# Performance work log

Measured on AMD Instinct MI355X. Metric: run time of the kernel, lower is better.

Reference implementation:

```python
import jax, jax.numpy as jnp
import numpy as np

TOP_K = 2


def setup_inputs() -> dict:
    key = jax.random.key(0)
    ks = jax.random.split(key, 6)
    B, S, H, I, E = 2, 1024, 1024, 2048, 8
    s_h = 1.0 / np.sqrt(H)
    s_i = 1.0 / np.sqrt(I)
    return {
        "x": jax.random.normal(ks[0], (B, S, H), jnp.float32),
        "gate_w": jax.random.normal(ks[1], (H, E), jnp.float32) * s_h,
        "gate_b": jnp.zeros((E,), jnp.float32),
        "w1": jax.random.normal(ks[2], (E, H, I), jnp.float32) * s_h,
        "w3": jax.random.normal(ks[3], (E, H, I), jnp.float32) * s_h,
        "w2": jax.random.normal(ks[4], (E, I, H), jnp.float32) * s_i,
    }


def reference(x, gate_w, gate_b, w1, w3, w2):
    # Gating: softmax over experts, then top-k selection + renormalization.
    logits = jnp.einsum("bsh,he->bse", x, gate_w) + gate_b            # [B,S,E]
    probs = jax.nn.softmax(logits, axis=-1)
    topk_w, topk_idx = jax.lax.top_k(probs, TOP_K)                    # [B,S,K]
    topk_w = topk_w / jnp.sum(topk_w, axis=-1, keepdims=True)

    E = gate_w.shape[-1]
    # Per-token combine weight for each expert (0 if not routed there).
    # one_hot: [B,S,K,E] -> combine: [B,S,E]
    combine = jnp.sum(jax.nn.one_hot(topk_idx, E, dtype=x.dtype) * topk_w[..., None], axis=-2)

    # SwiGLU expert FFN: down(silu(gate(x)) * up(x)); dense-masked reference
    # (compute every expert on every token, weight by combine; math identical
    # to the original gather/scatter loop since combine is 0 off-route).
    out = jnp.zeros_like(x)
    for e in range(E):
        h = jax.nn.silu(x @ w1[e]) * (x @ w3[e])                      # [B,S,I]
        out = out + combine[..., e:e + 1] * (h @ w2[e])               # [B,S,H]
    return out
```

## Files before the change

### kernel.cpp

```cpp
#include <hip/hip_runtime.h>
#include <hip/hip_bf16.h>
#include <math.h>

typedef __attribute__((ext_vector_type(4))) float f32x4;
typedef __attribute__((ext_vector_type(8))) short bf16x8;

#define T_TOK 2048
#define H_DIM 1024
#define I_DIM 2048
#define E_NUM 8

__device__ inline unsigned short f2bf(float f) {
  union { float f; unsigned int u; } v; v.f = f;
  unsigned int r = v.u + 0x7fffu + ((v.u >> 16) & 1u);
  return (unsigned short)(r >> 16);
}
__device__ inline unsigned int pack2(float a, float b) {
  return (unsigned int)f2bf(a) | ((unsigned int)f2bf(b) << 16);
}

__device__ inline void gld16(const void* g, void* l) {
  __builtin_amdgcn_global_load_lds((const __attribute__((address_space(1))) void*)g,
                                   (__attribute__((address_space(3))) void*)l, 16, 0, 0);
}

__device__ inline void transpose_pair(const float* __restrict__ ip, unsigned short* __restrict__ op,
                                      int R, int C, int rp, int ct, char* smem)
{
  unsigned short (*tl)[66] = (unsigned short (*)[66])smem;
  int r0 = rp * 128, c0 = ct * 64;
  int tid = threadIdx.x;
  int rq = (tid >> 4) * 4;
  int c4 = (tid & 15) * 4;
  const float* b0 = ip + (size_t)(r0 + rq) * C + c0 + c4;
  const float* b1 = b0 + (size_t)64 * C;
  float4 v[8];
  v[0] = *(const float4*)(b0);
  v[1] = *(const float4*)(b0 + C);
  v[2] = *(const float4*)(b0 + 2 * C);
  v[3] = *(const float4*)(b0 + 3 * C);
  v[4] = *(const float4*)(b1);
  v[5] = *(const float4*)(b1 + C);
  v[6] = *(const float4*)(b1 + 2 * C);
  v[7] = *(const float4*)(b1 + 3 * C);
  const float* f = (const float*)v;
#pragma unroll
  for (int j = 0; j < 4; ++j) {
    *(unsigned int*)&tl[c4 + j][rq]          = pack2(f[0 * 4 + j], f[1 * 4 + j]);
    *(unsigned int*)&tl[c4 + j][rq + 2]      = pack2(f[2 * 4 + j], f[3 * 4 + j]);
    *(unsigned int*)&tl[64 + c4 + j][rq]     = pack2(f[4 * 4 + j], f[5 * 4 + j]);
    *(unsigned int*)&tl[64 + c4 + j][rq + 2] = pack2(f[6 * 4 + j], f[7 * 4 + j]);
  }
  __syncthreads();
  int c = tid >> 3, r8 = (tid & 7) * 8;
#pragma unroll
  for (int it = 0; it < 2; ++it) {
    int cc = c + it * 32;
#pragma unroll
    for (int p = 0; p < 2; ++p) {
      uint4 o;
      o.x = *(const unsigned int*)&tl[p * 64 + cc][r8];
      o.y = *(const unsigned int*)&tl[p * 64 + cc][r8 + 2];
      o.z = *(const unsigned int*)&tl[p * 64 + cc][r8 + 4];
      o.w = *(const unsigned int*)&tl[p * 64 + cc][r8 + 6];
      *(uint4*)(op + (size_t)(c0 + cc) * R + r0 + p * 64 + r8) = o;
    }
  }
}

__global__ __launch_bounds__(256) void gate_t13(
    const float* __restrict__ x, const float* __restrict__ gw, const float* __restrict__ gb,
    int* __restrict__ rec_e, float* __restrict__ rec_w, unsigned short* __restrict__ xb,
    const float* __restrict__ w1, const float* __restrict__ w3,
    unsigned short* __restrict__ w1t, unsigned short* __restrict__ w3t)
{
  __shared__ __align__(16) char smem[128 * 66 * 2];
  int bx = blockIdx.x;
  if (bx >= 512) {
    int idx = bx - 512;
    int m = idx >> 8;
    int t8 = idx & 255;
    int rp = t8 & 7;
    int ct = t8 >> 3;
    const float* ip = (m < 8 ? w1 : w3) + (size_t)(m & 7) * ((size_t)H_DIM * I_DIM);
    unsigned short* op = (m < 8 ? w1t : w3t) + (size_t)(m & 7) * ((size_t)H_DIM * I_DIM);
    transpose_pair(ip, op, H_DIM, I_DIM, rp, ct, smem);
    return;
  }
  int wv = threadIdx.x >> 6, lane = threadIdx.x & 63;
  int t = bx * 4 + wv;
  const float* xr = x + (size_t)t * H_DIM;
  unsigned short* xo = xb + (size_t)t * H_DIM;
  float acc[8];
#pragma unroll
  for (int e = 0; e < 8; ++e) acc[e] = 0.f;
  for (int i = 0; i < H_DIM / 64; ++i) {
    int h = i * 64 + lane;
    float xv = xr[h];
    xo[h] = f2bf(xv);
    const float4* g = (const float4*)(gw + (size_t)h * 8);
    float4 g0 = g[0], g1 = g[1];
    acc[0] += xv * g0.x; acc[1] += xv * g0.y; acc[2] += xv * g0.z; acc[3] += xv * g0.w;
    acc[4] += xv * g1.x; acc[5] += xv * g1.y; acc[6] += xv * g1.z; acc[7] += xv * g1.w;
  }
#pragma unroll
  for (int s = 1; s < 64; s <<= 1) {
#pragma unroll
    for (int e = 0; e < 8; ++e) acc[e] += __shfl_xor(acc[e], s);
  }
  if (lane == 0) {
    float l[8];
#pragma unroll
    for (int e = 0; e < 8; ++e) l[e] = acc[e] + gb[e];
    int e0 = 0;
    for (int e = 1; e < 8; ++e) if (l[e] > l[e0]) e0 = e;
    int e1 = (e0 == 0) ? 1 : 0;
    for (int e = 0; e < 8; ++e) if (e != e0 && l[e] > l[e1]) e1 = e;
    float w0 = 1.f / (1.f + expf(l[e1] - l[e0]));
    rec_e[t * 2]     = e0; rec_e[t * 2 + 1] = e1;
    rec_w[t * 2]     = w0; rec_w[t * 2 + 1] = 1.f - w0;
  }
}

__global__ __launch_bounds__(256) void route8(
    const int* __restrict__ rec_e, const float* __restrict__ rec_w,
    int* __restrict__ counts_g, int* __restrict__ list_tok, float* __restrict__ list_w)
{
  __shared__ int cnt[8];
  __shared__ int fill;
  int e = blockIdx.x;
  int tid = threadIdx.x;
  if (tid < 8) cnt[tid] = 0;
  if (tid == 0) fill = 0;
  __syncthreads();
  int e_loc[16];
  int c_loc[8];
#pragma unroll
  for (int k = 0; k < 8; ++k) c_loc[k] = 0;
#pragma unroll
  for (int it = 0; it < 16; ++it) {
    e_loc[it] = rec_e[it * 256 + tid] & 7;
    c_loc[e_loc[it]]++;
  }
#pragma unroll
  for (int k = 0; k < 8; ++k) if (c_loc[k]) atomicAdd(&cnt[k], c_loc[k]);
  __syncthreads();
  if (e == 0 && tid < 8) counts_g[tid] = cnt[tid];
  int base = 0;
#pragma unroll
  for (int k = 0; k < 8; ++k) if (k < e) base += cnt[k];
#pragma unroll
  for (int it = 0; it < 16; ++it) {
    if (e_loc[it] == e) {
      int i = it * 256 + tid;
      int pos = atomicAdd(&fill, 1);
      list_tok[base + pos] = i;
      list_w[base + pos]   = rec_w[i];
    }
  }
}

__global__ __launch_bounds__(256, 2) void gemm1_t2(
    const unsigned short* __restrict__ xb,
    const unsigned short* __restrict__ w1t,
    const unsigned short* __restrict__ w3t,
    const int* __restrict__ counts,
    const int* __restrict__ list_tok,
    unsigned short* __restrict__ hbuf,
    const float* __restrict__ w2,
    unsigned short* __restrict__ w2t)
{
  __shared__ __align__(16) char smem[49152];
  int bx = blockIdx.x;
  if (bx >= 4096) {
    int idx = bx - 4096;
    int e = idx >> 8;
    int t8 = idx & 255;
    int rp = t8 & 15;
    int ct = t8 >> 4;
    const float* ip = w2 + (size_t)e * ((size_t)H_DIM * I_DIM);
    unsigned short* op = w2t + (size_t)e * ((size_t)H_DIM * I_DIM);
    transpose_pair(ip, op, I_DIM, H_DIM, rp, ct, smem);
    return;
  }
  int e = bx >> 9;
  int y = (bx >> 4) & 31;
  int ix = bx & 15;
  int nbase = 0;
#pragma unroll
  for (int i = 0; i < 8; ++i) if (i < e) nbase += counts[i];
  int n_e = counts[e];
  int t0 = y * 128;
  if (t0 >= n_e) return;
  int i0 = ix * 128;

  char* As  = smem;
  char* B1s = smem + 16384;
  char* B3s = smem + 32768;

  int tid = threadIdx.x;
  int r2 = tid >> 2;
  int seg = (tid & 3) * 8;

  int sr0 = t0 + r2;       if (sr0 >= n_e) sr0 = n_e - 1;
  int sr1 = t0 + 64 + r2;  if (sr1 >= n_e) sr1 = n_e - 1;
  int tok0 = list_tok[nbase + sr0] >> 1;
  int tok1 = list_tok[nbase + sr1] >> 1;
  const char* gA0 = (const char*)(xb + (size_t)tok0 * H_DIM + seg);
  const char* gA1 = (const char*)(xb + (size_t)tok1 * H_DIM + seg);
  const char* gB1a = (const char*)(w1t + ((size_t)e * I_DIM + i0 + r2) * H_DIM + seg);
  const char* gB1b = (const char*)(w1t + ((size_t)e * I_DIM + i0 + 64 + r2) * H_DIM + seg);
  const char* gB3a = (const char*)(w3t + ((size_t)e * I_DIM + i0 + r2) * H_DIM + seg);
  const char* gB3b = (const char*)(w3t + ((size_t)e * I_DIM + i0 + 64 + r2) * H_DIM + seg);

  int w = tid >> 6, lane = tid & 63, lm = lane & 15, lq = lane >> 4;
  int wm = w & 1, wn = w >> 1;

  f32x4 acc1[4][4], acc3[4][4];
#pragma unroll
  for (int i = 0; i < 4; ++i)
#pragma unroll
    for (int j = 0; j < 4; ++j) { acc1[i][j] = (f32x4){0,0,0,0}; acc3[i][j] = (f32x4){0,0,0,0}; }

  for (int kb = 0; kb < H_DIM; kb += 64) {
    __syncthreads();
    gld16(gA0 + kb * 2,       As + tid * 16);
    gld16(gA1 + kb * 2,       As + 4096 + tid * 16);
    gld16(gA0 + kb * 2 + 64,  As + 8192 + tid * 16);
    gld16(gA1 + kb * 2 + 64,  As + 12288 + tid * 16);
    gld16(gB1a + kb * 2,      B1s + tid * 16);
    gld16(gB1b + kb * 2,      B1s + 4096 + tid * 16);
    gld16(gB1a + kb * 2 + 64, B1s + 8192 + tid * 16);
    gld16(gB1b + kb * 2 + 64, B1s + 12288 + tid * 16);
    gld16(gB3a + kb * 2,      B3s + tid * 16);
    gld16(gB3b + kb * 2,      B3s + 4096 + tid * 16);
    gld16(gB3a + kb * 2 + 64, B3s + 8192 + tid * 16);
    gld16(gB3b + kb * 2 + 64, B3s + 12288 + tid * 16);
    __syncthreads();
#pragma unroll
    for (int s = 0; s < 2; ++s) {
      bf16x8 a[4], b1[4], b3[4];
#pragma unroll
      for (int i = 0; i < 4; ++i)
        a[i] = *(const bf16x8*)(As + s * 8192 + ((wm * 64 + i * 16 + lm) * 32 + lq * 8) * 2);
#pragma unroll
      for (int j = 0; j < 4; ++j) {
        b1[j] = *(const bf16x8*)(B1s + s * 8192 + ((wn * 64 + j * 16 + lm) * 32 + lq * 8) * 2);
        b3[j] = *(const bf16x8*)(B3s + s * 8192 + ((wn * 64 + j * 16 + lm) * 32 + lq * 8) * 2);
      }
#pragma unroll
      for (int i = 0; i < 4; ++i)
#pragma unroll
        for (int j = 0; j < 4; ++j) {
          acc1[i][j] = __builtin_amdgcn_mfma_f32_16x16x32_bf16(a[i], b1[j], acc1[i][j], 0, 0, 0);
          acc3[i][j] = __builtin_amdgcn_mfma_f32_16x16x32_bf16(a[i], b3[j], acc3[i][j], 0, 0, 0);
        }
    }
  }

#pragma unroll
  for (int i = 0; i < 4; ++i) {
#pragma unroll
    for (int rr = 0; rr < 4; ++rr) {
      int slot = t0 + wm * 64 + i * 16 + lq * 4 + rr;
      if (slot < n_e) {
        unsigned short* orow = hbuf + (size_t)(nbase + slot) * I_DIM + i0 + wn * 64 + lm;
#pragma unroll
        for (int j = 0; j < 4; ++j) {
          float g = acc1[i][j][rr], u = acc3[i][j][rr];
          float hv = (g / (1.f + __expf(-g))) * u;
          orow[j * 16] = f2bf(hv);
        }
      }
    }
  }
}

__global__ __launch_bounds__(256, 4) void gemm2(
    const unsigned short* __restrict__ hbuf,
    const unsigned short* __restrict__ w2t,
    const int* __restrict__ counts,
    const int* __restrict__ list_tok,
    const float* __restrict__ list_w,
    float* __restrict__ partial)
{
  __shared__ __align__(16) char smem[24576];
  int e = blockIdx.z;
  int nbase = 0;
#pragma unroll
  for (int i = 0; i < 8; ++i) if (i < e) nbase += counts[i];
  int n_e = counts[e];
  int ts = blockIdx.y >> 1, kh = blockIdx.y & 1;
  int t0 = ts * 64;
  if (t0 >= n_e) return;
  int h0 = blockIdx.x * 128;
  int k0 = kh * (I_DIM / 2);

  char* As = smem;
  char* Bs = smem + 8192;

  int tid = threadIdx.x;
  int r2 = tid >> 2;
  int seg = (tid & 3) * 8;

  int sr = t0 + r2; if (sr >= n_e) sr = n_e - 1;
  const char* gA  = (const char*)(hbuf + (size_t)(nbase + sr) * I_DIM + k0 + seg);
  const char* gB0 = (const char*)(w2t + ((size_t)e * H_DIM + h0 + r2) * I_DIM + k0 + seg);
  const char* gB1 = (const char*)(w2t + ((size_t)e * H_DIM + h0 + 64 + r2) * I_DIM + k0 + seg);

  int w = tid >> 6, lane = tid & 63, lm = lane & 15, lq = lane >> 4;
  int wm = w & 1, wn = (w >> 1) * 64;

  f32x4 acc[2][4];
#pragma unroll
  for (int i = 0; i < 2; ++i)
#pragma unroll
    for (int j = 0; j < 4; ++j) acc[i][j] = (f32x4){0,0,0,0};

  for (int kb = 0; kb < I_DIM / 2; kb += 64) {
    __syncthreads();
    gld16(gA + kb * 2,       As + tid * 16);
    gld16(gA + kb * 2 + 64,  As + 4096 + tid * 16);
    gld16(gB0 + kb * 2,      Bs + tid * 16);
    gld16(gB1 + kb * 2,      Bs + 4096 + tid * 16);
    gld16(gB0 + kb * 2 + 64, Bs + 8192 + tid * 16);
    gld16(gB1 + kb * 2 + 64, Bs + 12288 + tid * 16);
    __syncthreads();
#pragma unroll
    for (int s = 0; s < 2; ++s) {
      bf16x8 a[2], b[4];
#pragma unroll
      for (int i = 0; i < 2; ++i)
        a[i] = *(const bf16x8*)(As + s * 4096 + ((wm * 32 + i * 16 + lm) * 32 + lq * 8) * 2);
#pragma unroll
      for (int j = 0; j < 4; ++j)
        b[j] = *(const bf16x8*)(Bs + s * 8192 + ((wn + j * 16 + lm) * 32 + lq * 8) * 2);
#pragma unroll
      for (int i = 0; i < 2; ++i)
#pragma unroll
        for (int j = 0; j < 4; ++j)
          acc[i][j] = __builtin_amdgcn_mfma_f32_16x16x32_bf16(a[i], b[j], acc[i][j], 0, 0, 0);
    }
  }

  int entv[2][4]; float wtv[2][4];
#pragma unroll
  for (int i = 0; i < 2; ++i)
#pragma unroll
    for (int rr = 0; rr < 4; ++rr) {
      int slot = t0 + wm * 32 + i * 16 + lq * 4 + rr;
      if (slot < n_e) { entv[i][rr] = list_tok[nbase + slot]; wtv[i][rr] = list_w[nbase + slot]; }
      else entv[i][rr] = -1;
    }
#pragma unroll
  for (int i = 0; i < 2; ++i)
#pragma unroll
    for (int j = 0; j < 4; ++j)
#pragma unroll
      for (int rr = 0; rr < 4; ++rr) {
        if (entv[i][rr] >= 0) {
          int t = entv[i][rr] >> 1, kk = entv[i][rr] & 1;
          int plane = kh * 2 + kk;
          partial[((size_t)plane * T_TOK + t) * H_DIM + h0 + wn + j * 16 + lm] =
              acc[i][j][rr] * wtv[i][rr];
        }
      }
}

__global__ __launch_bounds__(256) void combine4(const float* __restrict__ partial,
                                                float* __restrict__ out)
{
  const size_t P = (size_t)T_TOK * H_DIM;
  size_t i = (size_t)(blockIdx.x * 256 + threadIdx.x) * 4;
  float4 a = *(const float4*)(partial + i);
  float4 b = *(const float4*)(partial + P + i);
  float4 c = *(const float4*)(partial + 2 * P + i);
  float4 d = *(const float4*)(partial + 3 * P + i);
  float4 o;
  o.x = a.x + b.x + c.x + d.x;
  o.y = a.y + b.y + c.y + d.y;
  o.z = a.z + b.z + c.z + d.z;
  o.w = a.w + b.w + c.w + d.w;
  *(float4*)(out + i) = o;
}

extern "C" void kernel_launch(void* const* d_in, const int* in_sizes, int n_in,
                              void* d_out, int out_size, void* d_ws, size_t ws_size,
                              hipStream_t stream) {
  const float* x  = (const float*)d_in[0];
  const float* gw = (const float*)d_in[1];
  const float* gb = (const float*)d_in[2];
  const float* w1 = (const float*)d_in[3];
  const float* w3 = (const float*)d_in[4];
  const float* w2 = (const float*)d_in[5];
  float* out = (float*)d_out;

  char* ws = (char*)d_ws;
  int*   counts   = (int*)(ws);
  int*   rec_e    = (int*)(ws + 128);
  float* rec_w    = (float*)(ws + 16512);
  int*   list_tok = (int*)(ws + 32896);
  float* list_w   = (float*)(ws + 49280);
  const size_t MB = 1024ull * 1024ull;
  unsigned short* xb   = (unsigned short*)(ws + 1 * MB);
  unsigned short* w1t  = (unsigned short*)(ws + 5 * MB);
  float* partial       = (float*)(ws + 5 * MB);
  unsigned short* w3t  = (unsigned short*)(ws + 37 * MB);
  unsigned short* w2t  = (unsigned short*)(ws + 69 * MB);
  unsigned short* hbuf = (unsigned short*)(ws + 101 * MB);

  gate_t13<<<512 + 4096, 256, 0, stream>>>(x, gw, gb, rec_e, rec_w, xb, w1, w3, w1t, w3t);
  route8<<<8, 256, 0, stream>>>(rec_e, rec_w, counts, list_tok, list_w);
  gemm1_t2<<<4096 + 2048, 256, 0, stream>>>(xb, w1t, w3t, counts, list_tok, hbuf, w2, w2t);
  gemm2<<<dim3(H_DIM / 128, 64, E_NUM), 256, 0, stream>>>(hbuf, w2t, counts, list_tok, list_w, partial);
  combine4<<<(T_TOK * H_DIM) / (256 * 4), 256, 0, stream>>>(partial, out);
}
```

Baseline: 336.6 us.

## Interleave weight transposes with compute blocks and retile both expert GEMMs

Transpose blocks are now interleaved with the gating blocks and with the first-GEMM blocks, instead of being appended after them, so the conversion of the weights overlaps with useful work across the grid. The first GEMM now steps K by 32 with a halved LDS footprint, and its grid drops the token tiles no expert can fill. The second GEMM moves to 128x128 tiles with a four-way K split, and a combine pass sums eight partial planes. The aim is more data reuse per block and better overlap, at the price of twice as much partial-sum traffic in and out of global memory.

```diff
diff --git a/kernel.cpp b/kernel.cpp
--- a/kernel.cpp
+++ b/kernel.cpp
@@ -76,10 +76,10 @@
 {
   __shared__ __align__(16) char smem[128 * 66 * 2];
   int bx = blockIdx.x;
-  if (bx >= 512) {
-    int idx = bx - 512;
-    int m = idx >> 8;
-    int t8 = idx & 255;
+  if (bx % 9 != 8) {
+    int t = bx - bx / 9;
+    int m = t >> 8;
+    int t8 = t & 255;
     int rp = t8 & 7;
     int ct = t8 >> 3;
     const float* ip = (m < 8 ? w1 : w3) + (size_t)(m & 7) * ((size_t)H_DIM * I_DIM);
@@ -87,8 +87,9 @@
     transpose_pair(ip, op, H_DIM, I_DIM, rp, ct, smem);
     return;
   }
+  int gblk = bx / 9;
   int wv = threadIdx.x >> 6, lane = threadIdx.x & 63;
-  int t = bx * 4 + wv;
+  int t = gblk * 4 + wv;
   const float* xr = x + (size_t)t * H_DIM;
   unsigned short* xo = xb + (size_t)t * H_DIM;
   float acc[8];
@@ -170,12 +171,12 @@
     const float* __restrict__ w2,
     unsigned short* __restrict__ w2t)
 {
-  __shared__ __align__(16) char smem[49152];
+  __shared__ __align__(16) char smem[24576];
   int bx = blockIdx.x;
-  if (bx >= 4096) {
-    int idx = bx - 4096;
-    int e = idx >> 8;
-    int t8 = idx & 255;
+  if ((bx & 1) == 0) {
+    int t = bx >> 1;
+    int e = t >> 8;
+    int t8 = t & 255;
     int rp = t8 & 15;
     int ct = t8 >> 4;
     const float* ip = w2 + (size_t)e * ((size_t)H_DIM * I_DIM);
@@ -183,9 +184,10 @@
     transpose_pair(ip, op, I_DIM, H_DIM, rp, ct, smem);
     return;
   }
-  int e = bx >> 9;
-  int y = (bx >> 4) & 31;
-  int ix = bx & 15;
+  int g = bx >> 1;
+  int e = g >> 8;
+  int y = (g >> 4) & 15;
+  int ix = g & 15;
   int nbase = 0;
 #pragma unroll
   for (int i = 0; i < 8; ++i) if (i < e) nbase += counts[i];
@@ -194,24 +196,31 @@
   if (t0 >= n_e) return;
   int i0 = ix * 128;
 
-  char* As  = smem;
-  char* B1s = smem + 16384;
-  char* B3s = smem + 32768;
+  unsigned short* As  = (unsigned short*)smem;
+  unsigned short* B1s = (unsigned short*)(smem + 8192);
+  unsigned short* B3s = (unsigned short*)(smem + 16384);
 
   int tid = threadIdx.x;
-  int r2 = tid >> 2;
+  int r4 = tid >> 2;
   int seg = (tid & 3) * 8;
 
-  int sr0 = t0 + r2;       if (sr0 >= n_e) sr0 = n_e - 1;
-  int sr1 = t0 + 64 + r2;  if (sr1 >= n_e) sr1 = n_e - 1;
+  int sr0 = t0 + r4;       if (sr0 >= n_e) sr0 = n_e - 1;
+  int sr1 = t0 + 64 + r4;  if (sr1 >= n_e) sr1 = n_e - 1;
   int tok0 = list_tok[nbase + sr0] >> 1;
   int tok1 = list_tok[nbase + sr1] >> 1;
   const char* gA0 = (const char*)(xb + (size_t)tok0 * H_DIM + seg);
   const char* gA1 = (const char*)(xb + (size_t)tok1 * H_DIM + seg);
-  const char* gB1a = (const char*)(w1t + ((size_t)e * I_DIM + i0 + r2) * H_DIM + seg);
-  const char* gB1b = (const char*)(w1t + ((size_t)e * I_DIM + i0 + 64 + r2) * H_DIM + seg);
-  const char* gB3a = (const char*)(w3t + ((size_t)e * I_DIM + i0 + r2) * H_DIM + seg);
-  const char* gB3b = (const char*)(w3t + ((size_t)e * I_DIM + i0 + 64 + r2) * H_DIM + seg);
+  const char* gB1a = (const char*)(w1t + ((size_t)e * I_DIM + i0 + r4) * H_DIM + seg);
+  const char* gB1b = (const char*)(w1t + ((size_t)e * I_DIM + i0 + 64 + r4) * H_DIM + seg);
+  const char* gB3a = (const char*)(w3t + ((size_t)e * I_DIM + i0 + r4) * H_DIM + seg);
+  const char* gB3b = (const char*)(w3t + ((size_t)e * I_DIM + i0 + 64 + r4) * H_DIM + seg);
+
+  char* lA0  = (char*)As + tid * 16;
+  char* lA1  = (char*)As + 4096 + tid * 16;
+  char* lB1a = (char*)B1s + tid * 16;
+  char* lB1b = (char*)B1s + 4096 + tid * 16;
+  char* lB3a = (char*)B3s + tid * 16;
+  char* lB3b = (char*)B3s + 4096 + tid * 16;
 
   int w = tid >> 6, lane = tid & 63, lm = lane & 15, lq = lane >> 4;
   int wm = w & 1, wn = w >> 1;
@@ -222,40 +231,31 @@
 #pragma unroll
     for (int j = 0; j < 4; ++j) { acc1[i][j] = (f32x4){0,0,0,0}; acc3[i][j] = (f32x4){0,0,0,0}; }
 
-  for (int kb = 0; kb < H_DIM; kb += 64) {
+  for (int kb = 0; kb < H_DIM; kb += 32) {
     __syncthreads();
-    gld16(gA0 + kb * 2,       As + tid * 16);
-    gld16(gA1 + kb * 2,       As + 4096 + tid * 16);
-    gld16(gA0 + kb * 2 + 64,  As + 8192 + tid * 16);
-    gld16(gA1 + kb * 2 + 64,  As + 12288 + tid * 16);
-    gld16(gB1a + kb * 2,      B1s + tid * 16);
-    gld16(gB1b + kb * 2,      B1s + 4096 + tid * 16);
-    gld16(gB1a + kb * 2 + 64, B1s + 8192 + tid * 16);
-    gld16(gB1b + kb * 2 + 64, B1s + 12288 + tid * 16);
-    gld16(gB3a + kb * 2,      B3s + tid * 16);
-    gld16(gB3b + kb * 2,      B3s + 4096 + tid * 16);
-    gld16(gB3a + kb * 2 + 64, B3s + 8192 + tid * 16);
-    gld16(gB3b + kb * 2 + 64, B3s + 12288 + tid * 16);
+    gld16(gA0 + kb * 2, lA0);
+    gld16(gA1 + kb * 2, lA1);
+    gld16(gB1a + kb * 2, lB1a);
+    gld16(gB1b + kb * 2, lB1b);
+    gld16(gB3a + kb * 2, lB3a);
+    gld16(gB3b + kb * 2, lB3b);
     __syncthreads();
-#pragma unroll
-    for (int s = 0; s < 2; ++s) {
-      bf16x8 a[4], b1[4], b3[4];
-#pragma unroll
-      for (int i = 0; i < 4; ++i)
-        a[i] = *(const bf16x8*)(As + s * 8192 + ((wm * 64 + i * 16 + lm) * 32 + lq * 8) * 2);
+    bf16x8 a[4], b1[4], b3[4];
+#pragma unroll
+    for (int i = 0; i < 4; ++i)
+      a[i] = *(const bf16x8*)((const char*)As + 2 * ((wm * 64 + i * 16 + lm) * 32 + lq * 8));
+#pragma unroll
+    for (int j = 0; j < 4; ++j) {
+      b1[j] = *(const bf16x8*)((const char*)B1s + 2 * ((wn * 64 + j * 16 + lm) * 32 + lq * 8));
+      b3[j] = *(const bf16x8*)((const char*)B3s + 2 * ((wn * 64 + j * 16 + lm) * 32 + lq * 8));
+    }
+#pragma unroll
+    for (int i = 0; i < 4; ++i)
 #pragma unroll
       for (int j = 0; j < 4; ++j) {
-        b1[j] = *(const bf16x8*)(B1s + s * 8192 + ((wn * 64 + j * 16 + lm) * 32 + lq * 8) * 2);
-        b3[j] = *(const bf16x8*)(B3s + s * 8192 + ((wn * 64 + j * 16 + lm) * 32 + lq * 8) * 2);
+        acc1[i][j] = __builtin_amdgcn_mfma_f32_16x16x32_bf16(a[i], b1[j], acc1[i][j], 0, 0, 0);
+        acc3[i][j] = __builtin_amdgcn_mfma_f32_16x16x32_bf16(a[i], b3[j], acc3[i][j], 0, 0, 0);
       }
-#pragma unroll
-      for (int i = 0; i < 4; ++i)
-#pragma unroll
-        for (int j = 0; j < 4; ++j) {
-          acc1[i][j] = __builtin_amdgcn_mfma_f32_16x16x32_bf16(a[i], b1[j], acc1[i][j], 0, 0, 0);
-          acc3[i][j] = __builtin_amdgcn_mfma_f32_16x16x32_bf16(a[i], b3[j], acc3[i][j], 0, 0, 0);
-        }
-    }
   }
 
 #pragma unroll
@@ -267,8 +267,8 @@
         unsigned short* orow = hbuf + (size_t)(nbase + slot) * I_DIM + i0 + wn * 64 + lm;
 #pragma unroll
         for (int j = 0; j < 4; ++j) {
-          float g = acc1[i][j][rr], u = acc3[i][j][rr];
-          float hv = (g / (1.f + __expf(-g))) * u;
+          float gg = acc1[i][j][rr], u = acc3[i][j][rr];
+          float hv = (gg / (1.f + __expf(-gg))) * u;
           orow[j * 16] = f2bf(hv);
         }
       }
@@ -276,7 +276,7 @@
   }
 }
 
-__global__ __launch_bounds__(256, 4) void gemm2(
+__global__ __launch_bounds__(256, 2) void gemm2(
     const unsigned short* __restrict__ hbuf,
     const unsigned short* __restrict__ w2t,
     const int* __restrict__ counts,
@@ -284,76 +284,80 @@
     const float* __restrict__ list_w,
     float* __restrict__ partial)
 {
-  __shared__ __align__(16) char smem[24576];
+  __shared__ __align__(16) char smem[32768];
   int e = blockIdx.z;
   int nbase = 0;
 #pragma unroll
   for (int i = 0; i < 8; ++i) if (i < e) nbase += counts[i];
   int n_e = counts[e];
-  int ts = blockIdx.y >> 1, kh = blockIdx.y & 1;
-  int t0 = ts * 64;
+  int ts = blockIdx.y >> 2, kh = blockIdx.y & 3;
+  int t0 = ts * 128;
   if (t0 >= n_e) return;
   int h0 = blockIdx.x * 128;
-  int k0 = kh * (I_DIM / 2);
+  int k0 = kh * (I_DIM / 4);
 
   char* As = smem;
-  char* Bs = smem + 8192;
+  char* Bs = smem + 16384;
 
   int tid = threadIdx.x;
   int r2 = tid >> 2;
   int seg = (tid & 3) * 8;
 
-  int sr = t0 + r2; if (sr >= n_e) sr = n_e - 1;
-  const char* gA  = (const char*)(hbuf + (size_t)(nbase + sr) * I_DIM + k0 + seg);
+  int sr0 = t0 + r2;       if (sr0 >= n_e) sr0 = n_e - 1;
+  int sr1 = t0 + 64 + r2;  if (sr1 >= n_e) sr1 = n_e - 1;
+  const char* gA0 = (const char*)(hbuf + (size_t)(nbase + sr0) * I_DIM + k0 + seg);
+  const char* gA1 = (const char*)(hbuf + (size_t)(nbase + sr1) * I_DIM + k0 + seg);
   const char* gB0 = (const char*)(w2t + ((size_t)e * H_DIM + h0 + r2) * I_DIM + k0 + seg);
   const char* gB1 = (const char*)(w2t + ((size_t)e * H_DIM + h0 + 64 + r2) * I_DIM + k0 + seg);
 
   int w = tid >> 6, lane = tid & 63, lm = lane & 15, lq = lane >> 4;
-  int wm = w & 1, wn = (w >> 1) * 64;
-
-  f32x4 acc[2][4];
-#pragma unroll
-  for (int i = 0; i < 2; ++i)
+  int wm = w & 1, wn = w >> 1;
+
+  f32x4 acc[4][4];
+#pragma unroll
+  for (int i = 0; i < 4; ++i)
 #pragma unroll
     for (int j = 0; j < 4; ++j) acc[i][j] = (f32x4){0,0,0,0};
 
-  for (int kb = 0; kb < I_DIM / 2; kb += 64) {
+  for (int kb = 0; kb < I_DIM / 4; kb += 64) {
     __syncthreads();
-    gld16(gA + kb * 2,       As + tid * 16);
-    gld16(gA + kb * 2 + 64,  As + 4096 + tid * 16);
-    gld16(gB0 + kb * 2,      Bs + tid * 16);
-    gld16(gB1 + kb * 2,      Bs + 4096 + tid * 16);
-    gld16(gB0 + kb * 2 + 64, Bs + 8192 + tid * 16);
-    gld16(gB1 + kb * 2 + 64, Bs + 12288 + tid * 16);
+    gld16(gA0 + kb * 2,       As + tid * 16);
+    gld16(gA1 + kb * 2,       As + 4096 + tid * 16);
+    gld16(gA0 + kb * 2 + 64,  As + 8192 + tid * 16);
+    gld16(gA1 + kb * 2 + 64,  As + 12288 + tid * 16);
+    gld16(gB0 + kb * 2,       Bs + tid * 16);
+    gld16(gB1 + kb * 2,       Bs + 4096 + tid * 16);
+    gld16(gB0 + kb * 2 + 64,  Bs + 8192 + tid * 16);
+    gld16(gB1 + kb * 2 + 64,  Bs + 12288 + tid * 16);
     __syncthreads();
 #pragma unroll
     for (int s = 0; s < 2; ++s) {
-      bf16x8 a[2], b[4];
-#pragma unroll
-      for (int i = 0; i < 2; ++i)
-        a[i] = *(const bf16x8*)(As + s * 4096 + ((wm * 32 + i * 16 + lm) * 32 + lq * 8) * 2);
+      bf16x8 a[4], b[4];
+#pragma unroll
+      for (int i = 0; i < 4; ++i)
+        a[i] = *(const bf16x8*)(As + s * 8192 + ((wm * 64 + i * 16 + lm) * 32 + lq * 8) * 2);
 #pragma unroll
       for (int j = 0; j < 4; ++j)
-        b[j] = *(const bf16x8*)(Bs + s * 8192 + ((wn + j * 16 + lm) * 32 + lq * 8) * 2);
-#pragma unroll
-      for (int i = 0; i < 2; ++i)
+        b[j] = *(const bf16x8*)(Bs + s * 8192 + ((wn * 64 + j * 16 + lm) * 32 + lq * 8) * 2);
+#pragma unroll
+      for (int i = 0; i < 4; ++i)
 #pragma unroll
         for (int j = 0; j < 4; ++j)
           acc[i][j] = __builtin_amdgcn_mfma_f32_16x16x32_bf16(a[i], b[j], acc[i][j], 0, 0, 0);
     }
   }
 
-  int entv[2][4]; float wtv[2][4];
-#pragma unroll
-  for (int i = 0; i < 2; ++i)
+  int entv[4][4]; float wtv[4][4];
+#pragma unroll
+  for (int i = 0; i < 4; ++i)
 #pragma unroll
     for (int rr = 0; rr < 4; ++rr) {
-      int slot = t0 + wm * 32 + i * 16 + lq * 4 + rr;
+      int slot = t0 + wm * 64 + i * 16 + lq * 4 + rr;
       if (slot < n_e) { entv[i][rr] = list_tok[nbase + slot]; wtv[i][rr] = list_w[nbase + slot]; }
       else entv[i][rr] = -1;
     }
 #pragma unroll
-  for (int i = 0; i < 2; ++i)
+  for (int i = 0; i < 4; ++i)
 #pragma unroll
     for (int j = 0; j < 4; ++j)
 #pragma unroll
@@ -361,27 +365,24 @@
         if (entv[i][rr] >= 0) {
           int t = entv[i][rr] >> 1, kk = entv[i][rr] & 1;
           int plane = kh * 2 + kk;
-          partial[((size_t)plane * T_TOK + t) * H_DIM + h0 + wn + j * 16 + lm] =
+          partial[((size_t)plane * T_TOK + t) * H_DIM + h0 + wn * 64 + j * 16 + lm] =
               acc[i][j][rr] * wtv[i][rr];
         }
       }
 }
 
-__global__ __launch_bounds__(256) void combine4(const float* __restrict__ partial,
+__global__ __launch_bounds__(256) void combine8(const float* __restrict__ partial,
                                                 float* __restrict__ out)
 {
   const size_t P = (size_t)T_TOK * H_DIM;
   size_t i = (size_t)(blockIdx.x * 256 + threadIdx.x) * 4;
-  float4 a = *(const float4*)(partial + i);
-  float4 b = *(const float4*)(partial + P + i);
-  float4 c = *(const float4*)(partial + 2 * P + i);
-  float4 d = *(const float4*)(partial + 3 * P + i);
-  float4 o;
-  o.x = a.x + b.x + c.x + d.x;
-  o.y = a.y + b.y + c.y + d.y;
-  o.z = a.z + b.z + c.z + d.z;
-  o.w = a.w + b.w + c.w + d.w;
-  *(float4*)(out + i) = o;
+  float4 s = *(const float4*)(partial + i);
+#pragma unroll
+  for (int p = 1; p < 8; ++p) {
+    float4 v = *(const float4*)(partial + p * P + i);
+    s.x += v.x; s.y += v.y; s.z += v.z; s.w += v.w;
+  }
+  *(float4*)(out + i) = s;
 }
 
 extern "C" void kernel_launch(void* const* d_in, const int* in_sizes, int n_in,
@@ -409,9 +410,9 @@
   unsigned short* w2t  = (unsigned short*)(ws + 69 * MB);
   unsigned short* hbuf = (unsigned short*)(ws + 101 * MB);
 
-  gate_t13<<<512 + 4096, 256, 0, stream>>>(x, gw, gb, rec_e, rec_w, xb, w1, w3, w1t, w3t);
+  gate_t13<<<4608, 256, 0, stream>>>(x, gw, gb, rec_e, rec_w, xb, w1, w3, w1t, w3t);
   route8<<<8, 256, 0, stream>>>(rec_e, rec_w, counts, list_tok, list_w);
-  gemm1_t2<<<4096 + 2048, 256, 0, stream>>>(xb, w1t, w3t, counts, list_tok, hbuf, w2, w2t);
+  gemm1_t2<<<4096, 256, 0, stream>>>(xb, w1t, w3t, counts, list_tok, hbuf, w2, w2t);
   gemm2<<<dim3(H_DIM / 128, 64, E_NUM), 256, 0, stream>>>(hbuf, w2t, counts, list_tok, list_w, partial);
-  combine4<<<(T_TOK * H_DIM) / (256 * 4), 256, 0, stream>>>(partial, out);
-}
+  combine8<<<(T_TOK * H_DIM) / (256 * 4), 256, 0, stream>>>(partial, out);
+}
```

Measured after the change: 379.3 us. 1.13x slower.
